# Optimization experiments

Measured on AMD Instinct MI355X. Metric: run time of the kernel, lower is better.

The kernel has to match this reference:

```python
import jax, jax.numpy as jnp
import numpy as np

NC = 10        # output capsule classes
R = 2048       # num_routes (input capsules)
IN_DIM = 8
OUT_DIM = 16
ITERS = 3
EPS = 1e-8


def squash(s):
    # norm / (1 + norm^2 + eps) * s, over last dim
    norm = jnp.linalg.norm(s, axis=-1, keepdims=True)
    return norm / (1.0 + norm ** 2 + EPS) * s


def setup_inputs() -> dict:
    key = jax.random.key(0)
    k1, k2 = jax.random.split(key)
    x = jax.random.normal(k1, (256, R, IN_DIM), dtype=jnp.float32)
    # W ~ N(0,1) per reset_params
    W = jax.random.normal(k2, (R, IN_DIM, NC * OUT_DIM), dtype=jnp.float32)
    # routing logits b initialized to zeros
    b = jnp.zeros((R, NC), dtype=jnp.float32)
    return {"x": x, "W": W, "b": b}


def reference(x, W, b):
    B = x.shape[0]
    # u_hat: [B, R, NC, OUT_DIM] = x[b,r,:] @ W[r,:,:]
    u_hat = jnp.einsum('bri,rio->bro', x, W).reshape(B, R, NC, OUT_DIM)
    # initial coupling from learned logits b (softmax over classes)
    c = jax.nn.softmax(b, axis=-1)                      # [R, NC]
    s = jnp.sum(c[None, :, :, None] * u_hat, axis=1)    # [B, NC, OUT_DIM]
    v = squash(s)
    # dynamic routing
    bB = jnp.broadcast_to(b, (B, R, NC))
    for _ in range(ITERS):
        # agreement: dot(u_hat, v) over OUT_DIM
        bB = bB + jnp.sum(u_hat * v[:, None, :, :], axis=-1)   # [B, R, NC]
        c = jax.nn.softmax(bB, axis=-1)                          # [B, R, NC]
        s = jnp.sum(c[..., None] * u_hat, axis=1)                # [B, NC, OUT_DIM]
        v = squash(s)
    return v, c
```

## Files before the change

### kernel.cpp

```cpp
#include <hip/hip_runtime.h>
#include <hip/hip_fp16.h>
#include <cstdint>
#include <cstddef>


#define B_   256
#define R_   2048
#define NC_  10
#define OD_  16
#define IN_  8
#define BH_  128
#define UROW 80

__device__ __forceinline__ float rsum16(float x){
  x += __shfl_xor(x, 1, 16);
  x += __shfl_xor(x, 2, 16);
  x += __shfl_xor(x, 4, 16);
  x += __shfl_xor(x, 8, 16);
  return x;
}
__device__ __forceinline__ float rmax16(float x){
  x = fmaxf(x, __shfl_xor(x, 1, 16));
  x = fmaxf(x, __shfl_xor(x, 2, 16));
  x = fmaxf(x, __shfl_xor(x, 4, 16));
  x = fmaxf(x, __shfl_xor(x, 8, 16));
  return x;
}
__device__ __forceinline__ unsigned pack_f16(float a, float b){
  __half2 h = __floats2half2_rn(a, b);
  return *(unsigned*)&h;
}
__device__ __forceinline__ void unpack8(uint4 d, float* f){
  float2 t;
  t = __half22float2(*(__half2*)&d.x); f[0] = t.x; f[1] = t.y;
  t = __half22float2(*(__half2*)&d.y); f[2] = t.x; f[3] = t.y;
  t = __half22float2(*(__half2*)&d.z); f[4] = t.x; f[5] = t.y;
  t = __half22float2(*(__half2*)&d.w); f[6] = t.x; f[7] = t.y;
}

__global__ __launch_bounds__(256) void uhat_kernel(const float* __restrict__ x,
                                                   const float* __restrict__ W,
                                                   uint32_t* __restrict__ U,
                                                   int b0){
  const int r = blockIdx.x;
  __shared__ float Wl[IN_ * 160];
  __shared__ uint32_t St[256 * 44];
  {
    const float4* Wg = (const float4*)(W + (size_t)r * (IN_ * 160));
    float4* Wl4 = (float4*)Wl;
    for (int i = threadIdx.x; i < 320; i += 256) Wl4[i] = Wg[i];
  }
  __syncthreads();
  const int nh = threadIdx.x >> 7;
  const int bl = threadIdx.x & 127;
  const float4* xp = (const float4*)(x + ((size_t)(b0 + bl) * R_ + r) * IN_);
  float4 xa = xp[0], xb = xp[1];
  float xr[8] = {xa.x, xa.y, xa.z, xa.w, xb.x, xb.y, xb.z, xb.w};
  const float4* Wl4 = (const float4*)Wl;
  uint32_t res[40];
  #pragma unroll
  for (int co = 0; co < 20; ++co){
    float4 u = make_float4(0.f, 0.f, 0.f, 0.f);
    #pragma unroll
    for (int i = 0; i < 8; ++i){
      float4 w = Wl4[i * 40 + nh * 20 + co];
      u.x = fmaf(xr[i], w.x, u.x);
      u.y = fmaf(xr[i], w.y, u.y);
      u.z = fmaf(xr[i], w.z, u.z);
      u.w = fmaf(xr[i], w.w, u.w);
    }
    res[2 * co]     = pack_f16(u.x, u.y);
    res[2 * co + 1] = pack_f16(u.z, u.w);
  }
  {
    uint4* row = (uint4*)(St + threadIdx.x * 44);
    #pragma unroll
    for (int k = 0; k < 10; ++k)
      row[k] = make_uint4(res[4*k], res[4*k+1], res[4*k+2], res[4*k+3]);
  }
  __syncthreads();
  uint4* dst = (uint4*)(U + (size_t)r * (BH_ * UROW));
  #pragma unroll
  for (int k2 = 0; k2 < 10; ++k2){
    int f    = k2 * 256 + threadIdx.x;
    int tp   = f / 10;
    int kk   = f - tp * 10;
    int srow = (tp >> 1) + (tp & 1) * 128;
    dst[f] = *(const uint4*)(St + srow * 44 + kk * 4);
  }
}

template<int MODE>
__global__ __launch_bounds__(256) void pass_kernel(
    const uint32_t* __restrict__ U,
    const float*    __restrict__ b_in,
    float*          __restrict__ bB,
    const float*    __restrict__ s_prev,
    float*          __restrict__ s_out,
    int b0)
{
  const int bl = blockIdx.x >> 3;
  const int b  = b0 + bl;
  const int rc = blockIdx.x & 7;
  const int n  = threadIdx.x & 15;
  const int rs = threadIdx.x >> 4;
  const int nn = (n < NC_) ? n : (NC_ - 1);

  float vreg[16];
  if (MODE != 0){
    const float* sp = s_prev + b * 160 + nn * 16;
    float ss = 0.f;
    #pragma unroll
    for (int o = 0; o < 16; ++o){ float t = sp[o]; vreg[o] = t; ss = fmaf(t, t, ss); }
    float f = sqrtf(ss) / (1.f + ss + 1e-8f);
    #pragma unroll
    for (int o = 0; o < 16; ++o) vreg[o] *= f;
  }
  float acc[16];
  #pragma unroll
  for (int o = 0; o < 16; ++o) acc[o] = 0.f;

  const int r0 = rc * 256;
  for (int rr = 0; rr < 16; ++rr){
    const int r = r0 + rr * 16 + rs;
    const uint4* up = (const uint4*)(U + ((size_t)r * BH_ + bl) * UROW + n * 8);
    float uf[16];
    unpack8(up[0], uf);
    unpack8(up[1], uf + 8);
    const size_t rowg = (size_t)b * R_ + r;

    float c;
    if (MODE == 0){
      float bold = b_in[r * NC_ + nn];
      float bnew = (n < NC_) ? bold : -1e30f;
      float m = rmax16(bnew);
      float e = __expf(bnew - m);
      float sum = rsum16(e);
      c = e / sum;
    } else {
      float t = 0.f;
      #pragma unroll
      for (int o = 0; o < 16; ++o) t = fmaf(uf[o], vreg[o], t);
      float bold = (MODE == 1) ? b_in[r * NC_ + nn] : bB[rowg * NC_ + nn];
      float bnew = (n < NC_) ? (bold + t) : -1e30f;
      float m = rmax16(bnew);
      float e = __expf(bnew - m);
      float sum = rsum16(e);
      c = e / sum;
      if (MODE == 3){
        if (n < NC_) bB[rowg * NC_ + n] = c;
      } else {
        if (n < NC_) bB[rowg * NC_ + n] = bnew;
      }
    }
    #pragma unroll
    for (int o = 0; o < 16; ++o) acc[o] = fmaf(c, uf[o], acc[o]);
  }

  __shared__ float sd[16 * 16 * 17];
  #pragma unroll
  for (int o = 0; o < 16; ++o) sd[rs * 272 + n * 17 + o] = acc[o];
  __syncthreads();
  const int n2 = threadIdx.x >> 4;
  const int o2 = threadIdx.x & 15;
  if (n2 < NC_){
    float tot = 0.f;
    #pragma unroll
    for (int k = 0; k < 16; ++k) tot += sd[k * 272 + n2 * 17 + o2];
    atomicAdd(&s_out[b * 160 + n2 * 16 + o2], tot);
  }
}

__global__ __launch_bounds__(256) void squash_final(const float* __restrict__ s,
                                                    float* __restrict__ vout){
  int g = blockIdx.x * 256 + threadIdx.x;
  float xv = s[g];
  float ss = rsum16(xv * xv);
  float norm = sqrtf(ss);
  vout[g] = (norm / (1.f + ss + 1e-8f)) * xv;
}

extern "C" void kernel_launch(void* const* d_in, const int* in_sizes, int n_in,
                              void* d_out, int out_size, void* d_ws, size_t ws_size,
                              hipStream_t stream){
  const float* x    = (const float*)d_in[0];
  const float* W    = (const float*)d_in[1];
  const float* b_in = (const float*)d_in[2];
  float* out = (float*)d_out;
  float* out_v = out;
  float* bB    = out + 40960;

  char* w = (char*)d_ws;
  uint32_t* U = (uint32_t*)w;
  float* s0 = (float*)(w + 83886080);
  float* s1 = s0 + 40960;
  float* s2 = s1 + 40960;
  float* s3 = s2 + 40960;

  hipMemsetAsync(s0, 0, 4 * 40960 * sizeof(float), stream);
  for (int h = 0; h < 2; ++h){
    const int b0 = h * BH_;
    uhat_kernel<<<R_, 256, 0, stream>>>(x, W, U, b0);
    pass_kernel<0><<<1024, 256, 0, stream>>>(U, b_in, bB, s0, s0, b0);
    pass_kernel<1><<<1024, 256, 0, stream>>>(U, b_in, bB, s0, s1, b0);
    pass_kernel<2><<<1024, 256, 0, stream>>>(U, b_in, bB, s1, s2, b0);
    pass_kernel<3><<<1024, 256, 0, stream>>>(U, b_in, bB, s2, s3, b0);
  }
  squash_final<<<160, 256, 0, stream>>>(s3, out_v);
}
```

Measured before the change: 254.9 us.

## Recompute routing logits from summed squashed vectors instead of storing bB

Because the logits accumulate u_hat·v over iterations, the pass kernel now sums the squashed vectors of all previous iterations and computes the logit as b + u_hat·(v0+v1+...). This removes the read-modify-write of the per-batch logit array [B,R,NC] in iterations 1 and 2, and only the final softmax coefficients are written. It also doubles the grid to 2048 blocks with half the routes per block and skips U loads for the padding lanes. The cost is a few extra squash evaluations per thread and more atomics into s_out.

```diff
diff --git a/kernel.cpp b/kernel.cpp
--- a/kernel.cpp
+++ b/kernel.cpp
@@ -36,6 +36,16 @@
   t = __half22float2(*(__half2*)&d.y); f[2] = t.x; f[3] = t.y;
   t = __half22float2(*(__half2*)&d.z); f[4] = t.x; f[5] = t.y;
   t = __half22float2(*(__half2*)&d.w); f[6] = t.x; f[7] = t.y;
+}
+__device__ __forceinline__ void add_squash(float* vreg, const float* __restrict__ s,
+                                           int b, int nn){
+  const float* sp = s + b * 160 + nn * 16;
+  float t[16]; float ss = 0.f;
+  #pragma unroll
+  for (int o = 0; o < 16; ++o){ t[o] = sp[o]; ss = fmaf(t[o], t[o], ss); }
+  float f = sqrtf(ss) / (1.f + ss + 1e-8f);
+  #pragma unroll
+  for (int o = 0; o < 16; ++o) vreg[o] = fmaf(f, t[o], vreg[o]);
 }
 
 __global__ __launch_bounds__(256) void uhat_kernel(const float* __restrict__ x,
@@ -94,65 +104,55 @@
 __global__ __launch_bounds__(256) void pass_kernel(
     const uint32_t* __restrict__ U,
     const float*    __restrict__ b_in,
-    float*          __restrict__ bB,
-    const float*    __restrict__ s_prev,
+    float*          __restrict__ c_out,
+    const float*    __restrict__ s0,
+    const float*    __restrict__ s1,
+    const float*    __restrict__ s2,
     float*          __restrict__ s_out,
     int b0)
 {
-  const int bl = blockIdx.x >> 3;
+  const int bl = blockIdx.x >> 4;
   const int b  = b0 + bl;
-  const int rc = blockIdx.x & 7;
+  const int rc = blockIdx.x & 15;
   const int n  = threadIdx.x & 15;
   const int rs = threadIdx.x >> 4;
   const int nn = (n < NC_) ? n : (NC_ - 1);
 
   float vreg[16];
-  if (MODE != 0){
-    const float* sp = s_prev + b * 160 + nn * 16;
-    float ss = 0.f;
-    #pragma unroll
-    for (int o = 0; o < 16; ++o){ float t = sp[o]; vreg[o] = t; ss = fmaf(t, t, ss); }
-    float f = sqrtf(ss) / (1.f + ss + 1e-8f);
-    #pragma unroll
-    for (int o = 0; o < 16; ++o) vreg[o] *= f;
-  }
+  #pragma unroll
+  for (int o = 0; o < 16; ++o) vreg[o] = 0.f;
+  if (MODE >= 1) add_squash(vreg, s0, b, nn);
+  if (MODE >= 2) add_squash(vreg, s1, b, nn);
+  if (MODE >= 3) add_squash(vreg, s2, b, nn);
+
   float acc[16];
   #pragma unroll
   for (int o = 0; o < 16; ++o) acc[o] = 0.f;
 
-  const int r0 = rc * 256;
-  for (int rr = 0; rr < 16; ++rr){
+  const int r0 = rc * 128;
+  for (int rr = 0; rr < 8; ++rr){
     const int r = r0 + rr * 16 + rs;
-    const uint4* up = (const uint4*)(U + ((size_t)r * BH_ + bl) * UROW + n * 8);
     float uf[16];
-    unpack8(up[0], uf);
-    unpack8(up[1], uf + 8);
-    const size_t rowg = (size_t)b * R_ + r;
-
-    float c;
-    if (MODE == 0){
-      float bold = b_in[r * NC_ + nn];
-      float bnew = (n < NC_) ? bold : -1e30f;
-      float m = rmax16(bnew);
-      float e = __expf(bnew - m);
-      float sum = rsum16(e);
-      c = e / sum;
-    } else {
-      float t = 0.f;
+    #pragma unroll
+    for (int o = 0; o < 16; ++o) uf[o] = 0.f;
+    if (n < NC_){
+      const uint4* up = (const uint4*)(U + ((size_t)r * BH_ + bl) * UROW + n * 8);
+      uint4 ua = up[0], ub = up[1];
+      unpack8(ua, uf);
+      unpack8(ub, uf + 8);
+    }
+    float t = 0.f;
+    if (MODE != 0){
       #pragma unroll
       for (int o = 0; o < 16; ++o) t = fmaf(uf[o], vreg[o], t);
-      float bold = (MODE == 1) ? b_in[r * NC_ + nn] : bB[rowg * NC_ + nn];
-      float bnew = (n < NC_) ? (bold + t) : -1e30f;
-      float m = rmax16(bnew);
-      float e = __expf(bnew - m);
-      float sum = rsum16(e);
-      c = e / sum;
-      if (MODE == 3){
-        if (n < NC_) bB[rowg * NC_ + n] = c;
-      } else {
-        if (n < NC_) bB[rowg * NC_ + n] = bnew;
-      }
     }
+    float bold = b_in[r * NC_ + nn];
+    float bnew = (n < NC_) ? (bold + t) : -1e30f;
+    float m = rmax16(bnew);
+    float e = __expf(bnew - m);
+    float sum = rsum16(e);
+    float c = e / sum;
+    if (MODE == 3 && n < NC_) c_out[((size_t)b * R_ + r) * NC_ + n] = c;
     #pragma unroll
     for (int o = 0; o < 16; ++o) acc[o] = fmaf(c, uf[o], acc[o]);
   }
@@ -188,7 +188,7 @@
   const float* b_in = (const float*)d_in[2];
   float* out = (float*)d_out;
   float* out_v = out;
-  float* bB    = out + 40960;
+  float* c_out = out + 40960;
 
   char* w = (char*)d_ws;
   uint32_t* U = (uint32_t*)w;
@@ -201,10 +201,10 @@
   for (int h = 0; h < 2; ++h){
     const int b0 = h * BH_;
     uhat_kernel<<<R_, 256, 0, stream>>>(x, W, U, b0);
-    pass_kernel<0><<<1024, 256, 0, stream>>>(U, b_in, bB, s0, s0, b0);
-    pass_kernel<1><<<1024, 256, 0, stream>>>(U, b_in, bB, s0, s1, b0);
-    pass_kernel<2><<<1024, 256, 0, stream>>>(U, b_in, bB, s1, s2, b0);
-    pass_kernel<3><<<1024, 256, 0, stream>>>(U, b_in, bB, s2, s3, b0);
+    pass_kernel<0><<<2048, 256, 0, stream>>>(U, b_in, c_out, s0, s1, s2, s0, b0);
+    pass_kernel<1><<<2048, 256, 0, stream>>>(U, b_in, c_out, s0, s1, s2, s1, b0);
+    pass_kernel<2><<<2048, 256, 0, stream>>>(U, b_in, c_out, s0, s1, s2, s2, b0);
+    pass_kernel<3><<<2048, 256, 0, stream>>>(U, b_in, c_out, s0, s1, s2, s3, b0);
   }
   squash_final<<<160, 256, 0, stream>>>(s3, out_v);
 }
```

Result: slower. 298.1 us (+17.0%).

## Recompute u_hat per pass from x and W instead of materializing it

Applied to the files above, without the earlier changes.

Drops the fp16 u_hat buffer in workspace. Each routing pass now recomputes u_hat on the fly in fp32 from x staged in shared memory and W held in registers. The routing logits are rebuilt from b_in plus the dot of u_hat with the sum of the previous squashed outputs, so the per-batch logits tensor no longer has to be written and read between passes. Partial sums are accumulated in shared memory and split across two output halves to reduce atomic contention. This trades repeated arithmetic and heavy register use (launch bounds 256,2) for removing large global-memory traffic.

```diff
diff --git a/kernel.cpp b/kernel.cpp
--- a/kernel.cpp
+++ b/kernel.cpp
@@ -1,5 +1,4 @@
 #include <hip/hip_runtime.h>
-#include <hip/hip_fp16.h>
 #include <cstdint>
 #include <cstddef>
 
@@ -7,10 +6,8 @@
 #define B_   256
 #define R_   2048
 #define NC_  10
-#define OD_  16
-#define IN_  8
-#define BH_  128
-#define UROW 80
+
+typedef __attribute__((ext_vector_type(4))) float f32x4;
 
 __device__ __forceinline__ float rsum16(float x){
   x += __shfl_xor(x, 1, 16);
@@ -26,155 +23,156 @@
   x = fmaxf(x, __shfl_xor(x, 8, 16));
   return x;
 }
-__device__ __forceinline__ unsigned pack_f16(float a, float b){
-  __half2 h = __floats2half2_rn(a, b);
-  return *(unsigned*)&h;
-}
-__device__ __forceinline__ void unpack8(uint4 d, float* f){
-  float2 t;
-  t = __half22float2(*(__half2*)&d.x); f[0] = t.x; f[1] = t.y;
-  t = __half22float2(*(__half2*)&d.y); f[2] = t.x; f[3] = t.y;
-  t = __half22float2(*(__half2*)&d.z); f[4] = t.x; f[5] = t.y;
-  t = __half22float2(*(__half2*)&d.w); f[6] = t.x; f[7] = t.y;
-}
-
-__global__ __launch_bounds__(256) void uhat_kernel(const float* __restrict__ x,
-                                                   const float* __restrict__ W,
-                                                   uint32_t* __restrict__ U,
-                                                   int b0){
-  const int r = blockIdx.x;
-  __shared__ float Wl[IN_ * 160];
-  __shared__ uint32_t St[256 * 44];
-  {
-    const float4* Wg = (const float4*)(W + (size_t)r * (IN_ * 160));
-    float4* Wl4 = (float4*)Wl;
-    for (int i = threadIdx.x; i < 320; i += 256) Wl4[i] = Wg[i];
+
+template<int MODE>
+__global__ __launch_bounds__(256, 2) void route_pass(
+    const float* __restrict__ x,
+    const float* __restrict__ W,
+    const float* __restrict__ b_in,
+    float*       __restrict__ c_out,
+    const float* __restrict__ s0,
+    const float* __restrict__ s1,
+    const float* __restrict__ s2,
+    float*       __restrict__ s_out)
+{
+  const int t    = threadIdx.x;
+  const int blkr = blockIdx.x & 31;
+  const int bgrp = blockIdx.x >> 5;
+  const int b0   = bgrp * 16;
+  const int n    = t & 15;
+  const int grp  = t >> 4;
+  const int w    = t >> 6;
+  const int nn   = (n < NC_) ? n : (NC_ - 1);
+
+  __shared__ float xs[16 * 128];
+  __shared__ float vs[16 * 164];
+  __shared__ float sacc[4 * 16 * 164];
+
+  for (int idx = t; idx < 4 * 16 * 164; idx += 256) sacc[idx] = 0.f;
+
+  if (MODE >= 1 && n < NC_){
+    const int bloc = grp;
+    const float* sl[3] = {s0, s1, s2};
+    float vr[16];
+    #pragma unroll
+    for (int o = 0; o < 16; ++o) vr[o] = 0.f;
+    #pragma unroll
+    for (int j = 0; j < MODE; ++j){
+      const float* sp = sl[j] + (size_t)(b0 + bloc) * 160 + n * 16;
+      float row[16]; float ssq = 0.f;
+      #pragma unroll
+      for (int o = 0; o < 16; ++o){
+        float v2 = sp[o] + sp[40960 + o];
+        row[o] = v2; ssq = fmaf(v2, v2, ssq);
+      }
+      float f = sqrtf(ssq) / (1.f + ssq + 1e-8f);
+      #pragma unroll
+      for (int o = 0; o < 16; ++o) vr[o] = fmaf(f, row[o], vr[o]);
+    }
+    #pragma unroll
+    for (int o = 0; o < 16; ++o) vs[bloc * 164 + n * 16 + o] = vr[o];
   }
-  __syncthreads();
-  const int nh = threadIdx.x >> 7;
-  const int bl = threadIdx.x & 127;
-  const float4* xp = (const float4*)(x + ((size_t)(b0 + bl) * R_ + r) * IN_);
-  float4 xa = xp[0], xb = xp[1];
-  float xr[8] = {xa.x, xa.y, xa.z, xa.w, xb.x, xb.y, xb.z, xb.w};
-  const float4* Wl4 = (const float4*)Wl;
-  uint32_t res[40];
-  #pragma unroll
-  for (int co = 0; co < 20; ++co){
-    float4 u = make_float4(0.f, 0.f, 0.f, 0.f);
-    #pragma unroll
-    for (int i = 0; i < 8; ++i){
-      float4 w = Wl4[i * 40 + nh * 20 + co];
-      u.x = fmaf(xr[i], w.x, u.x);
-      u.y = fmaf(xr[i], w.y, u.y);
-      u.z = fmaf(xr[i], w.z, u.z);
-      u.w = fmaf(xr[i], w.w, u.w);
-    }
-    res[2 * co]     = pack_f16(u.x, u.y);
-    res[2 * co + 1] = pack_f16(u.z, u.w);
-  }
-  {
-    uint4* row = (uint4*)(St + threadIdx.x * 44);
-    #pragma unroll
-    for (int k = 0; k < 10; ++k)
-      row[k] = make_uint4(res[4*k], res[4*k+1], res[4*k+2], res[4*k+3]);
-  }
-  __syncthreads();
-  uint4* dst = (uint4*)(U + (size_t)r * (BH_ * UROW));
-  #pragma unroll
-  for (int k2 = 0; k2 < 10; ++k2){
-    int f    = k2 * 256 + threadIdx.x;
-    int tp   = f / 10;
-    int kk   = f - tp * 10;
-    int srow = (tp >> 1) + (tp & 1) * 128;
-    dst[f] = *(const uint4*)(St + srow * 44 + kk * 4);
-  }
-}
-
-template<int MODE>
-__global__ __launch_bounds__(256) void pass_kernel(
-    const uint32_t* __restrict__ U,
-    const float*    __restrict__ b_in,
-    float*          __restrict__ bB,
-    const float*    __restrict__ s_prev,
-    float*          __restrict__ s_out,
-    int b0)
-{
-  const int bl = blockIdx.x >> 3;
-  const int b  = b0 + bl;
-  const int rc = blockIdx.x & 7;
-  const int n  = threadIdx.x & 15;
-  const int rs = threadIdx.x >> 4;
-  const int nn = (n < NC_) ? n : (NC_ - 1);
-
-  float vreg[16];
-  if (MODE != 0){
-    const float* sp = s_prev + b * 160 + nn * 16;
-    float ss = 0.f;
-    #pragma unroll
-    for (int o = 0; o < 16; ++o){ float t = sp[o]; vreg[o] = t; ss = fmaf(t, t, ss); }
-    float f = sqrtf(ss) / (1.f + ss + 1e-8f);
-    #pragma unroll
-    for (int o = 0; o < 16; ++o) vreg[o] *= f;
-  }
-  float acc[16];
-  #pragma unroll
-  for (int o = 0; o < 16; ++o) acc[o] = 0.f;
-
-  const int r0 = rc * 256;
-  for (int rr = 0; rr < 16; ++rr){
-    const int r = r0 + rr * 16 + rs;
-    const uint4* up = (const uint4*)(U + ((size_t)r * BH_ + bl) * UROW + n * 8);
-    float uf[16];
-    unpack8(up[0], uf);
-    unpack8(up[1], uf + 8);
-    const size_t rowg = (size_t)b * R_ + r;
-
-    float c;
+
+  for (int rc4 = 0; rc4 < 4; ++rc4){
+    const int r0 = blkr * 64 + rc4 * 16;
+    const int r  = r0 + grp;
+    __syncthreads();
+    #pragma unroll
+    for (int k = 0; k < 2; ++k){
+      int f = k * 256 + t;
+      int bb = f >> 5, inner = f & 31;
+      ((uint4*)xs)[f] =
+        ((const uint4*)(x + ((size_t)(b0 + bb) * R_ + r0) * 8))[inner];
+    }
+    __syncthreads();
+
+    f32x4 w4[32];
+    {
+      const float* wp = W + (size_t)r * 1280 + nn * 16;
+      #pragma unroll
+      for (int i = 0; i < 8; ++i)
+        #pragma unroll
+        for (int q = 0; q < 4; ++q)
+          w4[i * 4 + q] = *(const f32x4*)(wp + i * 160 + q * 4);
+    }
+    const float binr = b_in[r * NC_ + nn];
+    float c0r = 0.f;
     if (MODE == 0){
-      float bold = b_in[r * NC_ + nn];
-      float bnew = (n < NC_) ? bold : -1e30f;
+      float bnew = (n < NC_) ? binr : -1e30f;
       float m = rmax16(bnew);
       float e = __expf(bnew - m);
       float sum = rsum16(e);
-      c = e / sum;
-    } else {
-      float t = 0.f;
-      #pragma unroll
-      for (int o = 0; o < 16; ++o) t = fmaf(uf[o], vreg[o], t);
-      float bold = (MODE == 1) ? b_in[r * NC_ + nn] : bB[rowg * NC_ + nn];
-      float bnew = (n < NC_) ? (bold + t) : -1e30f;
-      float m = rmax16(bnew);
-      float e = __expf(bnew - m);
-      float sum = rsum16(e);
-      c = e / sum;
-      if (MODE == 3){
-        if (n < NC_) bB[rowg * NC_ + n] = c;
+      c0r = e / sum;
+    }
+
+    for (int bi = 0; bi < 16; ++bi){
+      const int bloc = (grp + bi) & 15;
+      const f32x4* xp = (const f32x4*)(xs + bloc * 128 + grp * 8);
+      f32x4 xa = xp[0], xb = xp[1];
+      float xr[8] = {xa[0], xa[1], xa[2], xa[3], xb[0], xb[1], xb[2], xb[3]};
+      float u[16];
+      #pragma unroll
+      for (int o = 0; o < 16; ++o) u[o] = 0.f;
+      #pragma unroll
+      for (int i = 0; i < 8; ++i)
+        #pragma unroll
+        for (int o = 0; o < 16; ++o)
+          u[o] = fmaf(xr[i], w4[i * 4 + (o >> 2)][o & 3], u[o]);
+
+      float c;
+      if (MODE == 0){
+        c = c0r;
       } else {
-        if (n < NC_) bB[rowg * NC_ + n] = bnew;
+        const f32x4* vp = (const f32x4*)(vs + bloc * 164 + nn * 16);
+        float t0 = 0.f, t1 = 0.f, t2 = 0.f, t3 = 0.f;
+        f32x4 v0 = vp[0], v1 = vp[1], v2 = vp[2], v3 = vp[3];
+        #pragma unroll
+        for (int j = 0; j < 4; ++j){
+          t0 = fmaf(u[j],      v0[j], t0);
+          t1 = fmaf(u[4 + j],  v1[j], t1);
+          t2 = fmaf(u[8 + j],  v2[j], t2);
+          t3 = fmaf(u[12 + j], v3[j], t3);
+        }
+        float td = (t0 + t1) + (t2 + t3);
+        float bnew = (n < NC_) ? (binr + td) : -1e30f;
+        float m = rmax16(bnew);
+        float e = __expf(bnew - m);
+        float sum = rsum16(e);
+        c = e / sum;
+        if (MODE == 3 && n < NC_)
+          c_out[((size_t)(b0 + bloc) * R_ + r) * NC_ + n] = c;
       }
-    }
-    #pragma unroll
-    for (int o = 0; o < 16; ++o) acc[o] = fmaf(c, uf[o], acc[o]);
+      if (n < NC_){
+        f32x4* sp = (f32x4*)(sacc + w * 2624 + bloc * 164 + n * 16);
+        #pragma unroll
+        for (int q = 0; q < 4; ++q){
+          f32x4 sv = sp[q];
+          #pragma unroll
+          for (int j = 0; j < 4; ++j) sv[j] = fmaf(c, u[4 * q + j], sv[j]);
+          sp[q] = sv;
+        }
+      }
+    }
   }
-
-  __shared__ float sd[16 * 16 * 17];
-  #pragma unroll
-  for (int o = 0; o < 16; ++o) sd[rs * 272 + n * 17 + o] = acc[o];
   __syncthreads();
-  const int n2 = threadIdx.x >> 4;
-  const int o2 = threadIdx.x & 15;
-  if (n2 < NC_){
-    float tot = 0.f;
-    #pragma unroll
-    for (int k = 0; k < 16; ++k) tot += sd[k * 272 + n2 * 17 + o2];
-    atomicAdd(&s_out[b * 160 + n2 * 16 + o2], tot);
+  {
+    const int bloc = t >> 4, col = t & 15;
+    float* dst = s_out + (blkr & 1) * 40960 + (size_t)(b0 + bloc) * 160 + col;
+    #pragma unroll
+    for (int nf = 0; nf < NC_; ++nf){
+      float acc = 0.f;
+      #pragma unroll
+      for (int ww = 0; ww < 4; ++ww)
+        acc += sacc[ww * 2624 + bloc * 164 + nf * 16 + col];
+      atomicAdd(dst + nf * 16, acc);
+    }
   }
 }
 
 __global__ __launch_bounds__(256) void squash_final(const float* __restrict__ s,
                                                     float* __restrict__ vout){
   int g = blockIdx.x * 256 + threadIdx.x;
-  float xv = s[g];
+  float xv = s[g] + s[40960 + g];
   float ss = rsum16(xv * xv);
   float norm = sqrtf(ss);
   vout[g] = (norm / (1.f + ss + 1e-8f)) * xv;
@@ -188,23 +186,17 @@
   const float* b_in = (const float*)d_in[2];
   float* out = (float*)d_out;
   float* out_v = out;
-  float* bB    = out + 40960;
-
-  char* w = (char*)d_ws;
-  uint32_t* U = (uint32_t*)w;
-  float* s0 = (float*)(w + 83886080);
-  float* s1 = s0 + 40960;
-  float* s2 = s1 + 40960;
-  float* s3 = s2 + 40960;
-
-  hipMemsetAsync(s0, 0, 4 * 40960 * sizeof(float), stream);
-  for (int h = 0; h < 2; ++h){
-    const int b0 = h * BH_;
-    uhat_kernel<<<R_, 256, 0, stream>>>(x, W, U, b0);
-    pass_kernel<0><<<1024, 256, 0, stream>>>(U, b_in, bB, s0, s0, b0);
-    pass_kernel<1><<<1024, 256, 0, stream>>>(U, b_in, bB, s0, s1, b0);
-    pass_kernel<2><<<1024, 256, 0, stream>>>(U, b_in, bB, s1, s2, b0);
-    pass_kernel<3><<<1024, 256, 0, stream>>>(U, b_in, bB, s2, s3, b0);
-  }
+  float* c_out = out + 40960;
+
+  float* s0 = (float*)d_ws;
+  float* s1 = s0 + 2 * 40960;
+  float* s2 = s1 + 2 * 40960;
+  float* s3 = s2 + 2 * 40960;
+
+  hipMemsetAsync(s0, 0, 8 * 40960 * sizeof(float), stream);
+  route_pass<0><<<512, 256, 0, stream>>>(x, W, b_in, c_out, s0, s1, s2, s0);
+  route_pass<1><<<512, 256, 0, stream>>>(x, W, b_in, c_out, s0, s1, s2, s1);
+  route_pass<2><<<512, 256, 0, stream>>>(x, W, b_in, c_out, s0, s1, s2, s2);
+  route_pass<3><<<512, 256, 0, stream>>>(x, W, b_in, c_out, s0, s1, s2, s3);
   squash_final<<<160, 256, 0, stream>>>(s3, out_v);
 }
```

Result: slower. 330.4 us (+29.6%).
